# Performance work log

Measured on AMD Instinct MI355X. Metric: run time of the kernel, lower is better.

Reference implementation:

```python
import jax, jax.numpy as jnp
import numpy as np

E = 256
H = 512
LN_EPS = 1e-5
NORM_EPS = 1e-12


def setup_inputs() -> dict:
    key = jax.random.key(0)
    ks = jax.random.split(key, 8)
    B, N, M = 8, 128, 128
    track_features = jax.random.normal(ks[0], (B, N, E), dtype=jnp.float32)
    det_features = jax.random.normal(ks[1], (B, M, E), dtype=jnp.float32)
    # MLP params (torch Linear default init style: uniform, but values irrelevant for correctness harness)
    lim1 = 1.0 / np.sqrt(3 * E)
    W1 = jax.random.uniform(ks[2], (3 * E, H), minval=-lim1, maxval=lim1, dtype=jnp.float32)
    b1 = jax.random.uniform(ks[3], (H,), minval=-lim1, maxval=lim1, dtype=jnp.float32)
    gamma = jnp.ones((H,), dtype=jnp.float32)
    beta = jnp.zeros((H,), dtype=jnp.float32)
    lim2 = 1.0 / np.sqrt(H)
    W2 = jax.random.uniform(ks[4], (H, 1), minval=-lim2, maxval=lim2, dtype=jnp.float32)
    b2 = jax.random.uniform(ks[5], (1,), minval=-lim2, maxval=lim2, dtype=jnp.float32)
    return {"track_features": track_features, "det_features": det_features,
            "W1": W1, "b1": b1, "gamma": gamma, "beta": beta, "W2": W2, "b2": b2}


def _l2_normalize(x):
    # F.normalize(x, dim=-1): x / max(||x||_2, eps)
    n = jnp.sqrt(jnp.sum(x * x, axis=-1, keepdims=True))
    return x / jnp.maximum(n, NORM_EPS)


def reference(track_features, det_features, W1, b1, gamma, beta, W2, b2):
    t = _l2_normalize(track_features)   # (B, N, E)
    d = _l2_normalize(det_features)     # (B, M, E)
    tb = t[:, :, None, :]               # (B, N, 1, E)
    db = d[:, None, :, :]               # (B, 1, M, E)
    B, N, _ = t.shape
    M = d.shape[1]
    diff = jnp.abs(tb - db)                                  # (B, N, M, E)
    pair = jnp.concatenate([jnp.broadcast_to(tb, (B, N, M, E)),
                            jnp.broadcast_to(db, (B, N, M, E)),
                            diff], axis=-1)                  # (B, N, M, 3E)
    h = jnp.einsum('bnme,eh->bnmh', pair, W1) + b1           # (B, N, M, H)
    mu = jnp.mean(h, axis=-1, keepdims=True)
    var = jnp.mean((h - mu) ** 2, axis=-1, keepdims=True)
    h = (h - mu) * jax.lax.rsqrt(var + LN_EPS) * gamma + beta
    h = h * jax.nn.sigmoid(h)                                # SiLU
    out = jnp.einsum('bnmh,ho->bnmo', h, W2)[..., 0] + b2[0]  # (B, N, M)
    return out
```

## Files before the change

kernel.cpp:

```cpp
#include <hip/hip_runtime.h>
#include <hip/hip_bf16.h>
#include <cstdint>

typedef __bf16 bf16x8 __attribute__((ext_vector_type(8)));
typedef __bf16 bf16x2 __attribute__((ext_vector_type(2)));
typedef float f32x4 __attribute__((ext_vector_type(4)));
typedef float f32x2 __attribute__((ext_vector_type(2)));

#define E_DIM 256
#define H_DIM 512

static __device__ __forceinline__ unsigned pkbf(float a, float b) {
    bf16x2 h;
    h[0] = (__bf16)a;
    h[1] = (__bf16)b;
    return __builtin_bit_cast(unsigned, h);
}

__global__ __launch_bounds__(512, 2)
void prep_kernel(const float* __restrict__ track, const float* __restrict__ det,
                 const float* __restrict__ W1, const float* __restrict__ b1,
                 float* __restrict__ P, float* __restrict__ Q,
                 __bf16* __restrict__ W1cc, float* __restrict__ sclT,
                 float* __restrict__ sclD) {
    __shared__ __align__(16) __bf16 Ash[16 * 256];
    int tid = threadIdx.x;
    int blk = blockIdx.x;

    if (blk >= 256) {
        int u = (blk - 256) * 512 + tid;
        int j = u & 3;
        int h = (u >> 2) & 511;
        int c = u >> 11;
        const float* src = W1 + (size_t)(512 + c * 32 + j * 8) * H_DIM + h;
        uint4 v;
        v.x = pkbf(src[0],                 src[(size_t)1 * H_DIM]);
        v.y = pkbf(src[(size_t)2 * H_DIM], src[(size_t)3 * H_DIM]);
        v.z = pkbf(src[(size_t)4 * H_DIM], src[(size_t)5 * H_DIM]);
        v.w = pkbf(src[(size_t)6 * H_DIM], src[(size_t)7 * H_DIM]);
        *(uint4*)(W1cc + ((size_t)(c * 512 + h) * 32 + j * 8)) = v;
        return;
    }

    int lane = tid & 63;
    int wave = tid >> 6;
    int lq   = lane >> 4;
    int lc   = lane & 15;
    int l5   = lane & 31;

    int mat  = blk >> 7;
    int rowg = (blk >> 1) & 63;
    int half = blk & 1;
    int r0   = rowg * 16;
    int h0   = half * 256;
    const float* src = mat ? det : track;

    {
        int row = wave * 2 + (lane >> 5);
        const float* gp = src + (size_t)(r0 + row) * E_DIM + l5 * 8;
        float4 x0 = *(const float4*)gp;
        float4 x1 = *(const float4*)(gp + 4);
        float ss = x0.x*x0.x + x0.y*x0.y + x0.z*x0.z + x0.w*x0.w
                 + x1.x*x1.x + x1.y*x1.y + x1.z*x1.z + x1.w*x1.w;
#pragma unroll
        for (int off = 16; off > 0; off >>= 1) ss += __shfl_xor(ss, off);
        float st = 1.0f / fmaxf(sqrtf(ss), 1e-12f);
        if (half == 0 && l5 == 0) (mat ? sclD : sclT)[r0 + row] = st;
        uint4 v;
        v.x = pkbf(x0.x * st, x0.y * st);
        v.y = pkbf(x0.z * st, x0.w * st);
        v.z = pkbf(x1.x * st, x1.y * st);
        v.w = pkbf(x1.z * st, x1.w * st);
        int cc = l5 >> 2, j = l5 & 3;
        *(uint4*)&Ash[(size_t)(cc * 64 + j * 16 + row) * 8] = v;
    }
    __syncthreads();

    int hB = h0 + wave * 32 + lc;
    const float* wb = W1 + (size_t)(mat * 256) * H_DIM + hB;
    float wf[2][8];
#pragma unroll
    for (int ht = 0; ht < 2; ++ht)
#pragma unroll
        for (int i = 0; i < 8; ++i)
            wf[ht][i] = wb[(size_t)(lq * 8 + i) * H_DIM + ht * 16];

    f32x4 acc[2];
    acc[0] = (f32x4){0.f, 0.f, 0.f, 0.f};
    acc[1] = (f32x4){0.f, 0.f, 0.f, 0.f};

#pragma unroll
    for (int c = 0; c < 8; ++c) {
        bf16x8 cw[2];
#pragma unroll
        for (int ht = 0; ht < 2; ++ht) {
            uint4 u;
            u.x = pkbf(wf[ht][0], wf[ht][1]);
            u.y = pkbf(wf[ht][2], wf[ht][3]);
            u.z = pkbf(wf[ht][4], wf[ht][5]);
            u.w = pkbf(wf[ht][6], wf[ht][7]);
            cw[ht] = __builtin_bit_cast(bf16x8, u);
        }
        if (c < 7) {
            const float* nb = wb + (size_t)((c + 1) * 32 + lq * 8) * H_DIM;
#pragma unroll
            for (int ht = 0; ht < 2; ++ht)
#pragma unroll
                for (int i = 0; i < 8; ++i)
                    wf[ht][i] = nb[(size_t)i * H_DIM + ht * 16];
        }
        bf16x8 af = *(const bf16x8*)&Ash[(size_t)(c * 64 + lane) * 8];
#pragma unroll
        for (int ht = 0; ht < 2; ++ht)
            acc[ht] = __builtin_amdgcn_mfma_f32_16x16x32_bf16(cw[ht], af, acc[ht], 0, 0, 0);
    }

    float* dst = mat ? Q : P;
#pragma unroll
    for (int ht = 0; ht < 2; ++ht) {
        int h = h0 + wave * 32 + ht * 16 + lq * 4;
        f32x4 o = acc[ht];
        if (!mat) o += *(const f32x4*)&b1[h];
        *(f32x4*)&dst[(size_t)(r0 + lc) * H_DIM + h] = o;
    }
}

__global__ __launch_bounds__(512, 4)
void main_kernel(const float* __restrict__ track, const float* __restrict__ det,
                 const __bf16* __restrict__ W1cc,
                 const float* __restrict__ P, const float* __restrict__ Q,
                 const float* __restrict__ sclT, const float* __restrict__ sclD,
                 const float* __restrict__ gamma, const float* __restrict__ beta,
                 const float* __restrict__ W2, const float* __restrict__ b2,
                 float* __restrict__ out) {
    __shared__ __align__(16) char SMEM[46336];
    __bf16* Ash  = (__bf16*)SMEM;
    float*  LNr1 = (float*)(SMEM + 32768);
    float*  LNr2 = (float*)(SMEM + 35072);
    float*  Red2 = (float*)(SMEM + 37376);
    float*  MuS  = (float*)(SMEM + 39680);
    float*  RsS  = (float*)(SMEM + 39936);
    float*  Gs   = (float*)(SMEM + 40192);
    float*  Bs   = (float*)(SMEM + 42240);
    float*  Ws   = (float*)(SMEM + 44288);

    int tid  = threadIdx.x;
    int lane = tid & 63;
    int wave = tid >> 6;
    int lq   = lane >> 4;
    int lc   = lane & 15;

    int i   = blockIdx.x;
    int xcd = i & 7;
    int t8  = (i >> 3) & 31;
    int b   = i >> 8;
    int n0  = ((xcd >> 1) * 4 + (t8 >> 3)) * 8;
    int m0  = ((xcd & 1) * 8 + (t8 & 7)) * 8;
    int gn  = b * 128 + n0;
    int gm  = b * 128 + m0;

    float b2v = b2[0];
    Gs[tid] = gamma[tid];
    Bs[tid] = beta[tid];
    Ws[tid] = W2[tid];

    const uint4* Wg = (const uint4*)W1cc;
    int hb = wave * 64 + lc;
    bf16x8 bwA[4], bwB[4];
#pragma unroll
    for (int ht = 0; ht < 4; ++ht)
        bwA[ht] = __builtin_bit_cast(bf16x8, Wg[(hb + ht * 16) * 4 + lq]);

    int k0 = wave * 32 + lq * 8;
    int ml = lane & 7;
    float sd = sclD[gm + ml];
    const float* dr = det + (size_t)(gm + ml) * E_DIM + k0;
    float4 d0 = *(const float4*)dr;
    float4 d1 = *(const float4*)(dr + 4);
#pragma unroll
    for (int r = 0; r < 4; ++r) {
        int nl = r * 2 + (lc >> 3);
        float st = sclT[gn + nl];
        const float* tr = track + (size_t)(gn + nl) * E_DIM + k0;
        float4 t0 = *(const float4*)tr;
        float4 t1 = *(const float4*)(tr + 4);
        uint4 v;
        v.x = pkbf(fabsf(t0.x * st - d0.x * sd), fabsf(t0.y * st - d0.y * sd));
        v.y = pkbf(fabsf(t0.z * st - d0.z * sd), fabsf(t0.w * st - d0.w * sd));
        v.z = pkbf(fabsf(t1.x * st - d1.x * sd), fabsf(t1.y * st - d1.y * sd));
        v.w = pkbf(fabsf(t1.z * st - d1.z * sd), fabsf(t1.w * st - d1.w * sd));
        *(uint4*)&Ash[(size_t)(r * 512 + wave * 64 + lane) * 8] = v;
    }

    const float* Pb = P + (size_t)gn * H_DIM;
    const float* Qb = Q + (size_t)gm * H_DIM;
    f32x4 acc[4][4];
    {
        f32x4 qv[4];
#pragma unroll
        for (int ht = 0; ht < 4; ++ht)
            qv[ht] = *(const f32x4*)&Qb[(size_t)ml * H_DIM + wave * 64 + ht * 16 + lq * 4];
#pragma unroll
        for (int pt = 0; pt < 4; ++pt) {
            int n = pt * 2 + (lc >> 3);
#pragma unroll
            for (int ht = 0; ht < 4; ++ht) {
                f32x4 pv = *(const f32x4*)&Pb[(size_t)n * H_DIM + wave * 64 + ht * 16 + lq * 4];
                acc[pt][ht] = pv + qv[ht];
            }
        }
    }
    __syncthreads();

#pragma unroll 2
    for (int c = 0; c < 8; ++c) {
        bf16x8* cur = (c & 1) ? bwB : bwA;
        bf16x8* nxt = (c & 1) ? bwA : bwB;
        int c1 = (c + 1) & 7;
#pragma unroll
        for (int ht = 0; ht < 4; ++ht)
            nxt[ht] = __builtin_bit_cast(bf16x8, Wg[c1 * 2048 + (hb + ht * 16) * 4 + lq]);
#pragma unroll
        for (int pt = 0; pt < 4; ++pt) {
            bf16x8 af = *(const bf16x8*)&Ash[(size_t)((pt * 8 + c) * 64 + lane) * 8];
#pragma unroll
            for (int ht = 0; ht < 4; ++ht)
                acc[pt][ht] = __builtin_amdgcn_mfma_f32_16x16x32_bf16(cur[ht], af, acc[pt][ht], 0, 0, 0);
        }
    }

#pragma unroll
    for (int pt = 0; pt < 4; ++pt) {
        f32x2 s1v = (f32x2){0.f, 0.f}, s2v = (f32x2){0.f, 0.f};
#pragma unroll
        for (int ht = 0; ht < 4; ++ht) {
#pragma unroll
            for (int hf = 0; hf < 2; ++hf) {
                f32x2 v = (f32x2){acc[pt][ht][hf * 2], acc[pt][ht][hf * 2 + 1]};
                s1v += v;
                s2v += v * v;
            }
        }
        float s1 = s1v[0] + s1v[1];
        float s2 = s2v[0] + s2v[1];
        s1 += __shfl_xor(s1, 16); s2 += __shfl_xor(s2, 16);
        s1 += __shfl_xor(s1, 32); s2 += __shfl_xor(s2, 32);
        if (lq == 0) {
            LNr1[(pt * 16 + lc) * 9 + wave] = s1;
            LNr2[(pt * 16 + lc) * 9 + wave] = s2;
        }
    }
    __syncthreads();
    {
        int p = tid >> 3, w = tid & 7;
        float s1 = LNr1[p * 9 + w];
        float s2 = LNr2[p * 9 + w];
        s1 += __shfl_xor(s1, 1); s2 += __shfl_xor(s2, 1);
        s1 += __shfl_xor(s1, 2); s2 += __shfl_xor(s2, 2);
        s1 += __shfl_xor(s1, 4); s2 += __shfl_xor(s2, 4);
        if (w == 0) {
            float mu  = s1 * (1.0f / 512.0f);
            float var = s2 * (1.0f / 512.0f) - mu * mu;
            MuS[p] = mu;
            RsS[p] = rsqrtf(var + 1e-5f);
        }
    }
    __syncthreads();

    float mus[4], rss[4];
#pragma unroll
    for (int pt = 0; pt < 4; ++pt) { mus[pt] = MuS[pt * 16 + lc]; rss[pt] = RsS[pt * 16 + lc]; }
    f32x2 cav[4];
#pragma unroll
    for (int pt = 0; pt < 4; ++pt) cav[pt] = (f32x2){0.f, 0.f};
#pragma unroll
    for (int ht = 0; ht < 4; ++ht) {
        int h = wave * 64 + ht * 16 + lq * 4;
        f32x4 g  = *(const f32x4*)&Gs[h];
        f32x4 bb = *(const f32x4*)&Bs[h];
        f32x4 w  = *(const f32x4*)&Ws[h];
#pragma unroll
        for (int pt = 0; pt < 4; ++pt) {
            f32x2 mu2 = (f32x2){mus[pt], mus[pt]};
            f32x2 rs2 = (f32x2){rss[pt], rss[pt]};
#pragma unroll
            for (int hf = 0; hf < 2; ++hf) {
                f32x2 v  = (f32x2){acc[pt][ht][hf * 2], acc[pt][ht][hf * 2 + 1]};
                f32x2 gg = (f32x2){g[hf * 2],  g[hf * 2 + 1]};
                f32x2 bv = (f32x2){bb[hf * 2], bb[hf * 2 + 1]};
                f32x2 wv = (f32x2){w[hf * 2],  w[hf * 2 + 1]};
                f32x2 x  = (v - mu2) * rs2 * gg + bv;
                f32x2 e, sg;
                e[0]  = __expf(-x[0]);
                e[1]  = __expf(-x[1]);
                sg[0] = __builtin_amdgcn_rcpf(1.0f + e[0]);
                sg[1] = __builtin_amdgcn_rcpf(1.0f + e[1]);
                cav[pt] += x * sg * wv;
            }
        }
    }
#pragma unroll
    for (int pt = 0; pt < 4; ++pt) {
        float cg = cav[pt][0] + cav[pt][1];
        cg += __shfl_xor(cg, 16);
        cg += __shfl_xor(cg, 32);
        if (lq == 0) Red2[(pt * 16 + lc) * 9 + wave] = cg;
    }
    __syncthreads();
    {
        int p = tid >> 3, w = tid & 7;
        float cg = Red2[p * 9 + w];
        cg += __shfl_xor(cg, 1);
        cg += __shfl_xor(cg, 2);
        cg += __shfl_xor(cg, 4);
        if (w == 0)
            out[(size_t)(gn + (p >> 3)) * 128 + m0 + (p & 7)] = b2v + cg;
    }
}

extern "C" void kernel_launch(void* const* d_in, const int* in_sizes, int n_in,
                              void* d_out, int out_size, void* d_ws, size_t ws_size,
                              hipStream_t stream) {
    const float* track = (const float*)d_in[0];
    const float* det   = (const float*)d_in[1];
    const float* W1    = (const float*)d_in[2];
    const float* b1    = (const float*)d_in[3];
    const float* gamma = (const float*)d_in[4];
    const float* beta  = (const float*)d_in[5];
    const float* W2    = (const float*)d_in[6];
    const float* b2    = (const float*)d_in[7];
    float* out = (float*)d_out;

    char* ws = (char*)d_ws;
    float*  Pp   = (float*)(ws);
    float*  Qp   = (float*)(ws + (2u << 20));
    __bf16* W1cc = (__bf16*)(ws + (4u << 20));
    float*  sclT = (float*)(ws + (4u << 20) + (256u << 10));
    float*  sclD = (float*)(ws + (4u << 20) + (264u << 10));

    prep_kernel<<<288, 512, 0, stream>>>(track, det, W1, b1, Pp, Qp, W1cc, sclT, sclD);
    main_kernel<<<2048, 512, 0, stream>>>(track, det, W1cc, Pp, Qp, sclT, sclD,
                                          gamma, beta, W2, b2, out);
}
```

Before: 143.2 us.

## Double main-kernel tile to 128 pairs with 1024-thread blocks sharing W1 loads

Each block of the main kernel now covers an 8x16 tile of track/detection pairs using 1024 threads (16 waves), with two wave groups sharing each per-wave slice of W1 columns. That halves the block count and the per-pair global reads of the W1 diff weights and Q rows, at the cost of doubling shared memory and a launch bound of one block per CU. The LayerNorm affine step is also rewritten as a precomputed scale-and-shift so the SiLU epilogue does fewer operations.

```diff
diff --git a/kernel.cpp b/kernel.cpp
--- a/kernel.cpp
+++ b/kernel.cpp
@@ -125,7 +125,7 @@
     }
 }
 
-__global__ __launch_bounds__(512, 4)
+__global__ __launch_bounds__(1024, 1)
 void main_kernel(const float* __restrict__ track, const float* __restrict__ det,
                  const __bf16* __restrict__ W1cc,
                  const float* __restrict__ P, const float* __restrict__ Q,
@@ -133,63 +133,70 @@
                  const float* __restrict__ gamma, const float* __restrict__ beta,
                  const float* __restrict__ W2, const float* __restrict__ b2,
                  float* __restrict__ out) {
-    __shared__ __align__(16) char SMEM[46336];
+    __shared__ __align__(16) char SMEM[86528];
     __bf16* Ash  = (__bf16*)SMEM;
-    float*  LNr1 = (float*)(SMEM + 32768);
-    float*  LNr2 = (float*)(SMEM + 35072);
-    float*  Red2 = (float*)(SMEM + 37376);
-    float*  MuS  = (float*)(SMEM + 39680);
-    float*  RsS  = (float*)(SMEM + 39936);
-    float*  Gs   = (float*)(SMEM + 40192);
-    float*  Bs   = (float*)(SMEM + 42240);
-    float*  Ws   = (float*)(SMEM + 44288);
+    float*  LNr1 = (float*)(SMEM + 65536);
+    float*  LNr2 = (float*)(SMEM + 70144);
+    float*  Red2 = (float*)(SMEM + 74752);
+    float*  MuS  = (float*)(SMEM + 79360);
+    float*  RsS  = (float*)(SMEM + 79872);
+    float*  Gs   = (float*)(SMEM + 80384);
+    float*  Bs   = (float*)(SMEM + 82432);
+    float*  Ws   = (float*)(SMEM + 84480);
 
     int tid  = threadIdx.x;
     int lane = tid & 63;
     int wave = tid >> 6;
+    int wh   = wave & 7;
+    int wp   = wave >> 3;
     int lq   = lane >> 4;
     int lc   = lane & 15;
 
     int i   = blockIdx.x;
     int xcd = i & 7;
-    int t8  = (i >> 3) & 31;
-    int b   = i >> 8;
-    int n0  = ((xcd >> 1) * 4 + (t8 >> 3)) * 8;
-    int m0  = ((xcd & 1) * 8 + (t8 & 7)) * 8;
+    int r8  = (i >> 3) & 15;
+    int b   = i >> 7;
+    int n0  = (xcd * 2 + (r8 >> 3)) * 8;
+    int m0  = (r8 & 7) * 16;
     int gn  = b * 128 + n0;
     int gm  = b * 128 + m0;
 
     float b2v = b2[0];
-    Gs[tid] = gamma[tid];
-    Bs[tid] = beta[tid];
-    Ws[tid] = W2[tid];
+    if (tid < 512) {
+        Gs[tid] = gamma[tid];
+        Bs[tid] = beta[tid];
+        Ws[tid] = W2[tid];
+    }
 
     const uint4* Wg = (const uint4*)W1cc;
-    int hb = wave * 64 + lc;
+    int hb = wh * 64 + lc;
     bf16x8 bwA[4], bwB[4];
 #pragma unroll
     for (int ht = 0; ht < 4; ++ht)
         bwA[ht] = __builtin_bit_cast(bf16x8, Wg[(hb + ht * 16) * 4 + lq]);
 
-    int k0 = wave * 32 + lq * 8;
-    int ml = lane & 7;
-    float sd = sclD[gm + ml];
-    const float* dr = det + (size_t)(gm + ml) * E_DIM + k0;
-    float4 d0 = *(const float4*)dr;
-    float4 d1 = *(const float4*)(dr + 4);
-#pragma unroll
-    for (int r = 0; r < 4; ++r) {
-        int nl = r * 2 + (lc >> 3);
-        float st = sclT[gn + nl];
-        const float* tr = track + (size_t)(gn + nl) * E_DIM + k0;
-        float4 t0 = *(const float4*)tr;
-        float4 t1 = *(const float4*)(tr + 4);
-        uint4 v;
-        v.x = pkbf(fabsf(t0.x * st - d0.x * sd), fabsf(t0.y * st - d0.y * sd));
-        v.y = pkbf(fabsf(t0.z * st - d0.z * sd), fabsf(t0.w * st - d0.w * sd));
-        v.z = pkbf(fabsf(t1.x * st - d1.x * sd), fabsf(t1.y * st - d1.y * sd));
-        v.w = pkbf(fabsf(t1.z * st - d1.z * sd), fabsf(t1.w * st - d1.w * sd));
-        *(uint4*)&Ash[(size_t)(r * 512 + wave * 64 + lane) * 8] = v;
+    {
+        int cS = wave & 7;
+        int nh = wave >> 3;
+        int k0 = cS * 32 + lq * 8;
+        float sd = sclD[gm + lc];
+        const float* drp = det + (size_t)(gm + lc) * E_DIM + k0;
+        float4 d0 = *(const float4*)drp;
+        float4 d1 = *(const float4*)(drp + 4);
+#pragma unroll
+        for (int r = 0; r < 4; ++r) {
+            int nl = nh * 4 + r;
+            float st = sclT[gn + nl];
+            const float* trp = track + (size_t)(gn + nl) * E_DIM + k0;
+            float4 t0 = *(const float4*)trp;
+            float4 t1 = *(const float4*)(trp + 4);
+            uint4 v;
+            v.x = pkbf(fabsf(t0.x * st - d0.x * sd), fabsf(t0.y * st - d0.y * sd));
+            v.y = pkbf(fabsf(t0.z * st - d0.z * sd), fabsf(t0.w * st - d0.w * sd));
+            v.z = pkbf(fabsf(t1.x * st - d1.x * sd), fabsf(t1.y * st - d1.y * sd));
+            v.w = pkbf(fabsf(t1.z * st - d1.z * sd), fabsf(t1.w * st - d1.w * sd));
+            *(uint4*)&Ash[(size_t)((nl * 8 + cS) * 64 + lane) * 8] = v;
+        }
     }
 
     const float* Pb = P + (size_t)gn * H_DIM;
@@ -199,13 +206,13 @@
         f32x4 qv[4];
 #pragma unroll
         for (int ht = 0; ht < 4; ++ht)
-            qv[ht] = *(const f32x4*)&Qb[(size_t)ml * H_DIM + wave * 64 + ht * 16 + lq * 4];
+            qv[ht] = *(const f32x4*)&Qb[(size_t)lc * H_DIM + wh * 64 + ht * 16 + lq * 4];
 #pragma unroll
         for (int pt = 0; pt < 4; ++pt) {
-            int n = pt * 2 + (lc >> 3);
+            int n = wp * 4 + pt;
 #pragma unroll
             for (int ht = 0; ht < 4; ++ht) {
-                f32x4 pv = *(const f32x4*)&Pb[(size_t)n * H_DIM + wave * 64 + ht * 16 + lq * 4];
+                f32x4 pv = *(const f32x4*)&Pb[(size_t)n * H_DIM + wh * 64 + ht * 16 + lq * 4];
                 acc[pt][ht] = pv + qv[ht];
             }
         }
@@ -222,7 +229,7 @@
             nxt[ht] = __builtin_bit_cast(bf16x8, Wg[c1 * 2048 + (hb + ht * 16) * 4 + lq]);
 #pragma unroll
         for (int pt = 0; pt < 4; ++pt) {
-            bf16x8 af = *(const bf16x8*)&Ash[(size_t)((pt * 8 + c) * 64 + lane) * 8];
+            bf16x8 af = *(const bf16x8*)&Ash[(size_t)(((wp * 4 + pt) * 8 + c) * 64 + lane) * 8];
 #pragma unroll
             for (int ht = 0; ht < 4; ++ht)
                 acc[pt][ht] = __builtin_amdgcn_mfma_f32_16x16x32_bf16(cur[ht], af, acc[pt][ht], 0, 0, 0);
@@ -246,8 +253,9 @@
         s1 += __shfl_xor(s1, 16); s2 += __shfl_xor(s2, 16);
         s1 += __shfl_xor(s1, 32); s2 += __shfl_xor(s2, 32);
         if (lq == 0) {
-            LNr1[(pt * 16 + lc) * 9 + wave] = s1;
-            LNr2[(pt * 16 + lc) * 9 + wave] = s2;
+            int p = wp * 64 + pt * 16 + lc;
+            LNr1[p * 9 + wh] = s1;
+            LNr2[p * 9 + wh] = s2;
         }
     }
     __syncthreads();
@@ -267,35 +275,41 @@
     }
     __syncthreads();
 
-    float mus[4], rss[4];
-#pragma unroll
-    for (int pt = 0; pt < 4; ++pt) { mus[pt] = MuS[pt * 16 + lc]; rss[pt] = RsS[pt * 16 + lc]; }
+    float as[4], bs[4];
+#pragma unroll
+    for (int pt = 0; pt < 4; ++pt) {
+        int p = wp * 64 + pt * 16 + lc;
+        float rs = RsS[p];
+        as[pt] = rs;
+        bs[pt] = -MuS[p] * rs;
+    }
     f32x2 cav[4];
 #pragma unroll
     for (int pt = 0; pt < 4; ++pt) cav[pt] = (f32x2){0.f, 0.f};
 #pragma unroll
     for (int ht = 0; ht < 4; ++ht) {
-        int h = wave * 64 + ht * 16 + lq * 4;
+        int h = wh * 64 + ht * 16 + lq * 4;
         f32x4 g  = *(const f32x4*)&Gs[h];
         f32x4 bb = *(const f32x4*)&Bs[h];
         f32x4 w  = *(const f32x4*)&Ws[h];
 #pragma unroll
         for (int pt = 0; pt < 4; ++pt) {
-            f32x2 mu2 = (f32x2){mus[pt], mus[pt]};
-            f32x2 rs2 = (f32x2){rss[pt], rss[pt]};
+            f32x2 a2 = (f32x2){as[pt], as[pt]};
+            f32x2 b2p = (f32x2){bs[pt], bs[pt]};
 #pragma unroll
             for (int hf = 0; hf < 2; ++hf) {
                 f32x2 v  = (f32x2){acc[pt][ht][hf * 2], acc[pt][ht][hf * 2 + 1]};
                 f32x2 gg = (f32x2){g[hf * 2],  g[hf * 2 + 1]};
                 f32x2 bv = (f32x2){bb[hf * 2], bb[hf * 2 + 1]};
                 f32x2 wv = (f32x2){w[hf * 2],  w[hf * 2 + 1]};
-                f32x2 x  = (v - mu2) * rs2 * gg + bv;
+                f32x2 x  = (v * a2 + b2p) * gg + bv;
+                f32x2 xw = x * wv;
                 f32x2 e, sg;
                 e[0]  = __expf(-x[0]);
                 e[1]  = __expf(-x[1]);
                 sg[0] = __builtin_amdgcn_rcpf(1.0f + e[0]);
                 sg[1] = __builtin_amdgcn_rcpf(1.0f + e[1]);
-                cav[pt] += x * sg * wv;
+                cav[pt] += xw * sg;
             }
         }
     }
@@ -304,7 +318,7 @@
         float cg = cav[pt][0] + cav[pt][1];
         cg += __shfl_xor(cg, 16);
         cg += __shfl_xor(cg, 32);
-        if (lq == 0) Red2[(pt * 16 + lc) * 9 + wave] = cg;
+        if (lq == 0) Red2[(wp * 64 + pt * 16 + lc) * 9 + wh] = cg;
     }
     __syncthreads();
     {
@@ -314,7 +328,7 @@
         cg += __shfl_xor(cg, 2);
         cg += __shfl_xor(cg, 4);
         if (w == 0)
-            out[(size_t)(gn + (p >> 3)) * 128 + m0 + (p & 7)] = b2v + cg;
+            out[(size_t)(gn + (p >> 4)) * 128 + m0 + (p & 15)] = b2v + cg;
     }
 }
 
@@ -339,6 +353,6 @@
     float*  sclD = (float*)(ws + (4u << 20) + (264u << 10));
 
     prep_kernel<<<288, 512, 0, stream>>>(track, det, W1, b1, Pp, Qp, W1cc, sclT, sclD);
-    main_kernel<<<2048, 512, 0, stream>>>(track, det, W1cc, Pp, Qp, sclT, sclD,
-                                          gamma, beta, W2, b2, out);
+    main_kernel<<<1024, 1024, 0, stream>>>(track, det, W1cc, Pp, Qp, sclT, sclD,
+                                           gamma, beta, W2, b2, out);
 }
```

New measurement: 153.5 us. 1.07x slower.

## Replace final block reduction with atomics, add MFMA priority, fold LN affine

Applied to the files above, without the earlier changes.

The final cross-wave reduction through shared memory and its barrier is replaced by per-wave atomicAdd into the output, which prep_kernel now zeroes using extra blocks. s_setprio raises wave priority around the MFMA loop, and the layernorm is rewritten as a multiply-add using precomputed rs and -mu*rs. This removes one __syncthreads and some LDS traffic, but adds 8 atomics per output, makes the float summation order nondeterministic, and adds a zeroing pass.

```diff
diff --git a/kernel.cpp b/kernel.cpp
--- a/kernel.cpp
+++ b/kernel.cpp
@@ -22,11 +22,19 @@
                  const float* __restrict__ W1, const float* __restrict__ b1,
                  float* __restrict__ P, float* __restrict__ Q,
                  __bf16* __restrict__ W1cc, float* __restrict__ sclT,
-                 float* __restrict__ sclD) {
+                 float* __restrict__ sclD, float* __restrict__ out) {
     __shared__ __align__(16) __bf16 Ash[16 * 256];
     int tid = threadIdx.x;
     int blk = blockIdx.x;
 
+    if (blk >= 288) {
+        int u = (blk - 288) * 512 + tid;
+        float4 z = {0.f, 0.f, 0.f, 0.f};
+#pragma unroll
+        for (int i = 0; i < 4; ++i)
+            ((float4*)out)[u + 8192 * i] = z;
+        return;
+    }
     if (blk >= 256) {
         int u = (blk - 256) * 512 + tid;
         int j = u & 3;
@@ -133,16 +141,15 @@
                  const float* __restrict__ gamma, const float* __restrict__ beta,
                  const float* __restrict__ W2, const float* __restrict__ b2,
                  float* __restrict__ out) {
-    __shared__ __align__(16) char SMEM[46336];
+    __shared__ __align__(16) char SMEM[44032];
     __bf16* Ash  = (__bf16*)SMEM;
     float*  LNr1 = (float*)(SMEM + 32768);
     float*  LNr2 = (float*)(SMEM + 35072);
-    float*  Red2 = (float*)(SMEM + 37376);
-    float*  MuS  = (float*)(SMEM + 39680);
-    float*  RsS  = (float*)(SMEM + 39936);
-    float*  Gs   = (float*)(SMEM + 40192);
-    float*  Bs   = (float*)(SMEM + 42240);
-    float*  Ws   = (float*)(SMEM + 44288);
+    float*  AS   = (float*)(SMEM + 37376);
+    float*  BS   = (float*)(SMEM + 37632);
+    float*  Gs   = (float*)(SMEM + 37888);
+    float*  Bs   = (float*)(SMEM + 39936);
+    float*  Ws   = (float*)(SMEM + 41984);
 
     int tid  = threadIdx.x;
     int lane = tid & 63;
@@ -220,6 +227,7 @@
 #pragma unroll
         for (int ht = 0; ht < 4; ++ht)
             nxt[ht] = __builtin_bit_cast(bf16x8, Wg[c1 * 2048 + (hb + ht * 16) * 4 + lq]);
+        __builtin_amdgcn_s_setprio(1);
 #pragma unroll
         for (int pt = 0; pt < 4; ++pt) {
             bf16x8 af = *(const bf16x8*)&Ash[(size_t)((pt * 8 + c) * 64 + lane) * 8];
@@ -227,6 +235,7 @@
             for (int ht = 0; ht < 4; ++ht)
                 acc[pt][ht] = __builtin_amdgcn_mfma_f32_16x16x32_bf16(cur[ht], af, acc[pt][ht], 0, 0, 0);
         }
+        __builtin_amdgcn_s_setprio(0);
     }
 
 #pragma unroll
@@ -261,15 +270,16 @@
         if (w == 0) {
             float mu  = s1 * (1.0f / 512.0f);
             float var = s2 * (1.0f / 512.0f) - mu * mu;
-            MuS[p] = mu;
-            RsS[p] = rsqrtf(var + 1e-5f);
+            float rs  = rsqrtf(var + 1e-5f);
+            AS[p] = rs;
+            BS[p] = -mu * rs;
         }
     }
     __syncthreads();
 
-    float mus[4], rss[4];
-#pragma unroll
-    for (int pt = 0; pt < 4; ++pt) { mus[pt] = MuS[pt * 16 + lc]; rss[pt] = RsS[pt * 16 + lc]; }
+    float as[4], bs[4];
+#pragma unroll
+    for (int pt = 0; pt < 4; ++pt) { as[pt] = AS[pt * 16 + lc]; bs[pt] = BS[pt * 16 + lc]; }
     f32x2 cav[4];
 #pragma unroll
     for (int pt = 0; pt < 4; ++pt) cav[pt] = (f32x2){0.f, 0.f};
@@ -281,21 +291,22 @@
         f32x4 w  = *(const f32x4*)&Ws[h];
 #pragma unroll
         for (int pt = 0; pt < 4; ++pt) {
-            f32x2 mu2 = (f32x2){mus[pt], mus[pt]};
-            f32x2 rs2 = (f32x2){rss[pt], rss[pt]};
+            f32x2 a2  = (f32x2){as[pt], as[pt]};
+            f32x2 b2p = (f32x2){bs[pt], bs[pt]};
 #pragma unroll
             for (int hf = 0; hf < 2; ++hf) {
                 f32x2 v  = (f32x2){acc[pt][ht][hf * 2], acc[pt][ht][hf * 2 + 1]};
                 f32x2 gg = (f32x2){g[hf * 2],  g[hf * 2 + 1]};
                 f32x2 bv = (f32x2){bb[hf * 2], bb[hf * 2 + 1]};
                 f32x2 wv = (f32x2){w[hf * 2],  w[hf * 2 + 1]};
-                f32x2 x  = (v - mu2) * rs2 * gg + bv;
+                f32x2 x  = (v * a2 + b2p) * gg + bv;
+                f32x2 xw = x * wv;
                 f32x2 e, sg;
                 e[0]  = __expf(-x[0]);
                 e[1]  = __expf(-x[1]);
                 sg[0] = __builtin_amdgcn_rcpf(1.0f + e[0]);
                 sg[1] = __builtin_amdgcn_rcpf(1.0f + e[1]);
-                cav[pt] += x * sg * wv;
+                cav[pt] += xw * sg;
             }
         }
     }
@@ -304,17 +315,12 @@
         float cg = cav[pt][0] + cav[pt][1];
         cg += __shfl_xor(cg, 16);
         cg += __shfl_xor(cg, 32);
-        if (lq == 0) Red2[(pt * 16 + lc) * 9 + wave] = cg;
-    }
-    __syncthreads();
-    {
-        int p = tid >> 3, w = tid & 7;
-        float cg = Red2[p * 9 + w];
-        cg += __shfl_xor(cg, 1);
-        cg += __shfl_xor(cg, 2);
-        cg += __shfl_xor(cg, 4);
-        if (w == 0)
-            out[(size_t)(gn + (p >> 3)) * 128 + m0 + (p & 7)] = b2v + cg;
+        if (lq == 0) {
+            if (wave == 0) cg += b2v;
+            int n = pt * 2 + (lc >> 3);
+            int m = lc & 7;
+            atomicAdd(&out[(size_t)(gn + n) * 128 + m0 + m], cg);
+        }
     }
 }
 
@@ -338,7 +344,7 @@
     float*  sclT = (float*)(ws + (4u << 20) + (256u << 10));
     float*  sclD = (float*)(ws + (4u << 20) + (264u << 10));
 
-    prep_kernel<<<288, 512, 0, stream>>>(track, det, W1, b1, Pp, Qp, W1cc, sclT, sclD);
+    prep_kernel<<<304, 512, 0, stream>>>(track, det, W1, b1, Pp, Qp, W1cc, sclT, sclD, out);
     main_kernel<<<2048, 512, 0, stream>>>(track, det, W1cc, Pp, Qp, sclT, sclD,
                                           gamma, beta, W2, b2, out);
 }
```

Measured after the change: 142.9 us. About the same (-0.2%).
